# Kernel optimization log

Hardware: AMD Instinct MI355X
Metric: run time of the kernel (lower is better)

Reference implementation:

```python
import jax, jax.numpy as jnp
import numpy as np

N = 100000   # nodes
E = 1600000  # edges
G = 512      # graphs in batch
F_IN = 128
H = 128
F_OUT = 1


def setup_inputs() -> dict:
    key = jax.random.key(0)
    ks = jax.random.split(key, 12)
    x = jax.random.normal(ks[0], (N, F_IN), dtype=jnp.float32)
    src = jax.random.randint(ks[1], (E,), 0, N, dtype=jnp.int32)
    dst = jax.random.randint(ks[2], (E,), 0, N, dtype=jnp.int32)
    node2graph = jnp.sort(jax.random.randint(ks[3], (N,), 0, G, dtype=jnp.int32))
    s_in = 1.0 / np.sqrt(F_IN)
    s_h = 1.0 / np.sqrt(H)
    W0 = jax.random.normal(ks[4], (F_IN, H), dtype=jnp.float32) * s_in
    b0 = jnp.zeros((H,), dtype=jnp.float32)
    W1 = jax.random.normal(ks[5], (H, H), dtype=jnp.float32) * s_h
    b1 = jnp.zeros((H,), dtype=jnp.float32)
    W2 = jax.random.normal(ks[6], (H, H), dtype=jnp.float32) * s_h
    b2 = jnp.zeros((H,), dtype=jnp.float32)
    Wm1 = jax.random.normal(ks[7], (H, H), dtype=jnp.float32) * s_h
    bm1 = jnp.zeros((H,), dtype=jnp.float32)
    Wm2 = jax.random.normal(ks[8], (H, F_OUT), dtype=jnp.float32) * s_h
    bm2 = jnp.zeros((F_OUT,), dtype=jnp.float32)
    return {"x": x, "src": src, "dst": dst, "node2graph": node2graph,
            "W0": W0, "b0": b0, "W1": W1, "b1": b1, "W2": W2, "b2": b2,
            "Wm1": Wm1, "bm1": bm1, "Wm2": Wm2, "bm2": bm2}


def _degree_norms(src, dst):
    ones = jnp.ones((E,), dtype=jnp.float32)
    out_deg = jax.ops.segment_sum(ones, src, num_segments=N)
    in_deg = jax.ops.segment_sum(ones, dst, num_segments=N)
    norm_out = jax.lax.rsqrt(jnp.maximum(out_deg, 1.0))  # [N]
    norm_in = jax.lax.rsqrt(jnp.maximum(in_deg, 1.0))    # [N]
    return norm_out, norm_in


def _graph_conv(x, src, dst, norm_out, norm_in, W, b):
    # DGL GraphConv, norm='both', in_feats <= out_feats path:
    # aggregate normalized src features, then linear + activation.
    xs = x * norm_out[:, None]
    msg = xs[src]                                         # [E, H] gather
    agg = jax.ops.segment_sum(msg, dst, num_segments=N)   # [N, H] scatter-add
    agg = agg * norm_in[:, None]
    return jax.nn.relu(agg @ W + b)


def reference(x, src, dst, node2graph, W0, b0, W1, b1, W2, b2, Wm1, bm1, Wm2, bm2):
    norm_out, norm_in = _degree_norms(src, dst)
    h = _graph_conv(x, src, dst, norm_out, norm_in, W0, b0)
    h = _graph_conv(h, src, dst, norm_out, norm_in, W1, b1)
    h = _graph_conv(h, src, dst, norm_out, norm_in, W2, b2)
    # sum_nodes readout per graph
    g = jax.ops.segment_sum(h, node2graph, num_segments=G)  # [G, H]
    # MLP head: Linear -> ReLU -> Linear
    return jax.nn.relu(g @ Wm1 + bm1) @ Wm2 + bm2           # [G, 1]
```

## Files before the change

kernel.cpp:

```cpp
#include <hip/hip_runtime.h>

#define NN 100000
#define NE 1600000
#define NG 512
#define HD 128

#define NBK 196
#define CHUNK 5120
#define NC 313
#define LH (2 * NBK * NC)

typedef _Float16 h8 __attribute__((ext_vector_type(8)));
typedef float f32x4 __attribute__((ext_vector_type(4)));

__global__ __launch_bounds__(512) void k_hist(const int* __restrict__ src,
                                              const int* __restrict__ dst,
                                              int* __restrict__ H,
                                              const float* __restrict__ W0,
                                              const float* __restrict__ W1,
                                              const float* __restrict__ W2,
                                              _Float16* __restrict__ Bt) {
    if (blockIdx.x >= NC) {
        int i = (blockIdx.x - NC) * 512 + threadIdx.x;
        int w = i >> 14;
        int rem = i & 16383;
        int n = rem >> 7;
        int k = rem & 127;
        const float* W = (w == 0) ? W0 : ((w == 1) ? W1 : W2);
        Bt[i] = (_Float16)W[k * 128 + n];
        return;
    }
    __shared__ int hd[NBK], hs[NBK];
    int c = blockIdx.x;
    for (int i = threadIdx.x; i < NBK; i += 512) { hd[i] = 0; hs[i] = 0; }
    __syncthreads();
    int e0 = c * CHUNK;
    int e1 = e0 + CHUNK; if (e1 > NE) e1 = NE;
    for (int e = e0 + threadIdx.x; e < e1; e += 512) {
        atomicAdd(&hd[dst[e] >> 9], 1);
        atomicAdd(&hs[src[e] >> 9], 1);
    }
    __syncthreads();
    for (int i = threadIdx.x; i < NBK; i += 512) {
        H[i * NC + c] = hd[i];
        H[NBK * NC + i * NC + c] = hs[i];
    }
}

__global__ __launch_bounds__(256) void k_scan1g(int* __restrict__ H,
                                                int* __restrict__ bsum, int L) {
    __shared__ int s[256];
    int i = blockIdx.x * 256 + threadIdx.x;
    int v = (i < L) ? H[i] : 0;
    s[threadIdx.x] = v;
    __syncthreads();
    for (int off = 1; off < 256; off <<= 1) {
        int t = (threadIdx.x >= off) ? s[threadIdx.x - off] : 0;
        __syncthreads();
        s[threadIdx.x] += t;
        __syncthreads();
    }
    if (i < L) H[i] = s[threadIdx.x] - v;
    if (threadIdx.x == 255) bsum[blockIdx.x] = s[255];
}

__global__ __launch_bounds__(256) void k_scan3g(int* __restrict__ H,
                                                const int* __restrict__ bsum,
                                                int L, int nb) {
    __shared__ int sb[512];
    __shared__ int tmp2[256];
    int t = threadIdx.x;
    int b0 = (2 * t < nb) ? bsum[2 * t] : 0;
    int b1 = (2 * t + 1 < nb) ? bsum[2 * t + 1] : 0;
    int pair = b0 + b1;
    tmp2[t] = pair;
    __syncthreads();
    for (int off = 1; off < 256; off <<= 1) {
        int v2 = (t >= off) ? tmp2[t - off] : 0;
        __syncthreads();
        tmp2[t] += v2;
        __syncthreads();
    }
    int ex = tmp2[t] - pair;
    sb[2 * t] = ex;
    sb[2 * t + 1] = ex + b0;
    __syncthreads();
    int i = blockIdx.x * 256 + t;
    if (i < L) H[i] += sb[i >> 8];
}

__global__ __launch_bounds__(512) void k_scatter(const int* __restrict__ src,
                                                 const int* __restrict__ dst,
                                                 const int* __restrict__ H,
                                                 int* __restrict__ dpart,
                                                 unsigned short* __restrict__ spart) {
    __shared__ int cd[NBK], cs[NBK];
    int c = blockIdx.x;
    for (int i = threadIdx.x; i < NBK; i += 512) {
        cd[i] = H[i * NC + c];
        cs[i] = H[NBK * NC + i * NC + c] - NE;
    }
    __syncthreads();
    int e0 = c * CHUNK;
    int e1 = e0 + CHUNK; if (e1 > NE) e1 = NE;
    for (int e = e0 + threadIdx.x; e < e1; e += 512) {
        int s = src[e], d = dst[e];
        int pd = atomicAdd(&cd[d >> 9], 1);
        dpart[pd] = s | ((d & 511) << 17);
        int ps = atomicAdd(&cs[s >> 9], 1);
        spart[ps] = (unsigned short)(s & 511);
    }
}

__global__ __launch_bounds__(512) void k_bucket(const int* __restrict__ dpart,
                                                const unsigned short* __restrict__ spart,
                                                const int* __restrict__ H,
                                                int* __restrict__ offs,
                                                int* __restrict__ csr,
                                                float* __restrict__ ni,
                                                float* __restrict__ no) {
    __shared__ int deg[512];
    __shared__ int cur[512];
    __shared__ int tmp[512];
    int b = blockIdx.x;
    bool isDst = (b < NBK);
    int bb = isDst ? b : b - NBK;
    int start, end;
    if (isDst) {
        start = H[bb * NC];
        end = (bb + 1 < NBK) ? H[(bb + 1) * NC] : NE;
    } else {
        start = H[NBK * NC + bb * NC] - NE;
        end = (bb + 1 < NBK) ? H[NBK * NC + (bb + 1) * NC] - NE : NE;
    }
    int t = threadIdx.x;
    deg[t] = 0;
    __syncthreads();
    if (isDst) {
        for (int i = start + t; i < end; i += 512)
            atomicAdd(&deg[(dpart[i] >> 17) & 511], 1);
    } else {
        for (int i = start + t; i < end; i += 512)
            atomicAdd(&deg[spart[i]], 1);
    }
    __syncthreads();
    int vb = bb * 512;
    if (!isDst) {
        int v = vb + t;
        if (v < NN) no[v] = rsqrtf(fmaxf((float)deg[t], 1.0f));
        return;
    }
    int a = deg[t];
    tmp[t] = a;
    __syncthreads();
    for (int off = 1; off < 512; off <<= 1) {
        int v2 = (t >= off) ? tmp[t - off] : 0;
        __syncthreads();
        tmp[t] += v2;
        __syncthreads();
    }
    cur[t] = start + tmp[t] - a;
    {
        int v = vb + t;
        if (v < NN) {
            offs[v] = cur[t];
            ni[v] = rsqrtf(fmaxf((float)a, 1.0f));
        }
    }
    if (b == NBK - 1 && t == 0) offs[NN] = NE;
    __syncthreads();
    for (int i = start + t; i < end; i += 512) {
        int pk = dpart[i];
        int p = atomicAdd(&cur[(pk >> 17) & 511], 1);
        csr[p] = pk & 0x1FFFF;
    }
}

template <typename TA>
__global__ __launch_bounds__(256) void k_gemm_mfma(const TA* __restrict__ A,
                                                   const _Float16* __restrict__ Bt,
                                                   const float* __restrict__ no,
                                                   _Float16* __restrict__ Zh,
                                                   int nrows) {
    __shared__ _Float16 Bs[128 * 136];
    int tid = threadIdx.x;
    {
        const h8* B8 = (const h8*)Bt;
        h8* Bs8 = (h8*)Bs;
        for (int i = tid; i < 2048; i += 256) {
            int n = i >> 4, c = i & 15;
            Bs8[n * 17 + c] = B8[i];
        }
    }

    int wave = tid >> 6;
    int lane = tid & 63;
    int m16 = lane & 15;
    int quad = lane >> 4;
    int rowbase = blockIdx.x * 64 + wave * 16;
    int row = rowbase + m16;
    bool valid = row < nrows;

    h8 afrag[4];
    if (valid) {
        if constexpr (sizeof(TA) == 2) {
            const h8* Arow = (const h8*)(A + (size_t)row * 128);
#pragma unroll
            for (int kk = 0; kk < 4; kk++) afrag[kk] = Arow[kk * 4 + quad];
        } else {
            const float4* Arow = (const float4*)(A + (size_t)row * 128);
#pragma unroll
            for (int kk = 0; kk < 4; kk++) {
                float4 lo = Arow[kk * 8 + quad * 2];
                float4 hi = Arow[kk * 8 + quad * 2 + 1];
                h8 a;
                a[0] = (_Float16)lo.x; a[1] = (_Float16)lo.y;
                a[2] = (_Float16)lo.z; a[3] = (_Float16)lo.w;
                a[4] = (_Float16)hi.x; a[5] = (_Float16)hi.y;
                a[6] = (_Float16)hi.z; a[7] = (_Float16)hi.w;
                afrag[kk] = a;
            }
        }
    } else {
#pragma unroll
        for (int kk = 0; kk < 4; kk++) {
            h8 a;
#pragma unroll
            for (int j = 0; j < 8; j++) a[j] = (_Float16)0.f;
            afrag[kk] = a;
        }
    }

    __syncthreads();

    f32x4 acc[8];
#pragma unroll
    for (int nt = 0; nt < 8; nt++) acc[nt] = (f32x4){0.f, 0.f, 0.f, 0.f};

    const h8* Bs8 = (const h8*)Bs;
#pragma unroll
    for (int nt = 0; nt < 8; nt++) {
        const h8* Bp = Bs8 + (size_t)(nt * 16 + m16) * 17;
#pragma unroll
        for (int kk = 0; kk < 4; kk++) {
            acc[nt] = __builtin_amdgcn_mfma_f32_16x16x32_f16(afrag[kk], Bp[kk * 4 + quad],
                                                             acc[nt], 0, 0, 0);
        }
    }

    float nor[4];
#pragma unroll
    for (int r = 0; r < 4; r++) {
        int grow = rowbase + quad * 4 + r;
        nor[r] = (grow < nrows) ? no[grow] : 0.f;
    }

    __syncthreads();
    {
        int lr0 = wave * 16 + quad * 4;
#pragma unroll
        for (int nt = 0; nt < 8; nt++) {
#pragma unroll
            for (int r = 0; r < 4; r++) {
                Bs[(size_t)(lr0 + r) * 136 + nt * 16 + m16] =
                    (_Float16)(acc[nt][r] * nor[r]);
            }
        }
    }
    __syncthreads();

    int blockrow0 = blockIdx.x * 64;
    for (int i = tid; i < 1024; i += 256) {
        int r = i >> 4, cch = i & 15;
        int grow = blockrow0 + r;
        if (grow < nrows) {
            h8 val = *(const h8*)&Bs[(size_t)r * 136 + cch * 8];
            *(h8*)&Zh[(size_t)grow * 128 + cch * 8] = val;
        }
    }
}

__global__ __launch_bounds__(256) void k_agg(const h8* __restrict__ Zh,
                                             const int* __restrict__ offs,
                                             const int* __restrict__ csr,
                                             const float* __restrict__ ni,
                                             const float* __restrict__ b,
                                             h8* __restrict__ H16) {
    int v = blockIdx.x * 16 + (threadIdx.x >> 4);
    int c = threadIdx.x & 15;
    int s = offs[v];
    int e = offs[v + 1];
    float a0[8], a1[8];
#pragma unroll
    for (int j = 0; j < 8; j++) { a0[j] = 0.f; a1[j] = 0.f; }
    int i = s;
    for (; i + 4 <= e; i += 4) {
        int u0 = csr[i];
        int u1 = csr[i + 1];
        int u2 = csr[i + 2];
        int u3 = csr[i + 3];
        h8 z0 = Zh[(size_t)u0 * 16 + c];
        h8 z1 = Zh[(size_t)u1 * 16 + c];
        h8 z2 = Zh[(size_t)u2 * 16 + c];
        h8 z3 = Zh[(size_t)u3 * 16 + c];
#pragma unroll
        for (int j = 0; j < 8; j++) {
            a0[j] += (float)z0[j] + (float)z1[j];
            a1[j] += (float)z2[j] + (float)z3[j];
        }
    }
    for (; i < e; i++) {
        int u = csr[i];
        h8 z = Zh[(size_t)u * 16 + c];
#pragma unroll
        for (int j = 0; j < 8; j++) a0[j] += (float)z[j];
    }
    float niv = ni[v];
    const float* bb = b + c * 8;
    h8 r;
#pragma unroll
    for (int j = 0; j < 8; j++)
        r[j] = (_Float16)fmaxf((a0[j] + a1[j]) * niv + bb[j], 0.f);
    H16[(size_t)v * 16 + c] = r;
}

__global__ __launch_bounds__(256) void k_readhead(const h8* __restrict__ H8,
                                                  const int* __restrict__ n2g,
                                                  const float* __restrict__ Wm1,
                                                  const float* __restrict__ bm1,
                                                  const float* __restrict__ Wm2,
                                                  const float* __restrict__ bm2,
                                                  float* __restrict__ out) {
    __shared__ float red[256 * 8];
    __shared__ float gs[128];
    __shared__ float red2[128];
    int gi = blockIdx.x;
    int t = threadIdx.x;
    int slot = t >> 4;
    int c = t & 15;

    int lo = 0, hi = NN;
    while (lo < hi) { int mid = (lo + hi) >> 1; if (n2g[mid] < gi) lo = mid + 1; else hi = mid; }
    int s = lo;
    hi = NN;
    while (lo < hi) { int mid = (lo + hi) >> 1; if (n2g[mid] < gi + 1) lo = mid + 1; else hi = mid; }
    int e = lo;

    float acc[8];
#pragma unroll
    for (int j = 0; j < 8; j++) acc[j] = 0.f;
    for (int v = s + slot; v < e; v += 16) {
        h8 z = H8[(size_t)v * 16 + c];
#pragma unroll
        for (int j = 0; j < 8; j++) acc[j] += (float)z[j];
    }
#pragma unroll
    for (int j = 0; j < 8; j++) red[t * 8 + j] = acc[j];
    __syncthreads();
    for (int off = 8; off >= 1; off >>= 1) {
        if (slot < off) {
#pragma unroll
            for (int j = 0; j < 8; j++)
                red[t * 8 + j] += red[(t + off * 16) * 8 + j];
        }
        __syncthreads();
    }
    if (slot == 0) {
#pragma unroll
        for (int j = 0; j < 8; j++) gs[c * 8 + j] = red[t * 8 + j];
    }
    __syncthreads();

    if (t < 128) {
        float a = bm1[t];
        for (int k = 0; k < 128; k++) a += gs[k] * Wm1[k * 128 + t];
        red2[t] = fmaxf(a, 0.f) * Wm2[t];
    }
    __syncthreads();
    for (int s2 = 64; s2 > 0; s2 >>= 1) {
        if (t < s2) red2[t] += red2[t + s2];
        __syncthreads();
    }
    if (t == 0) out[gi] = red2[0] + bm2[0];
}

extern "C" void kernel_launch(void* const* d_in, const int* in_sizes, int n_in,
                              void* d_out, int out_size, void* d_ws, size_t ws_size,
                              hipStream_t stream) {
    const float* x   = (const float*)d_in[0];
    const int*   src = (const int*)d_in[1];
    const int*   dst = (const int*)d_in[2];
    const int*   n2g = (const int*)d_in[3];
    const float* W0  = (const float*)d_in[4];
    const float* b0  = (const float*)d_in[5];
    const float* W1  = (const float*)d_in[6];
    const float* b1  = (const float*)d_in[7];
    const float* W2  = (const float*)d_in[8];
    const float* b2  = (const float*)d_in[9];
    const float* Wm1 = (const float*)d_in[10];
    const float* bm1 = (const float*)d_in[11];
    const float* Wm2 = (const float*)d_in[12];
    const float* bm2 = (const float*)d_in[13];
    float* out = (float*)d_out;

    char* p = (char*)d_ws;
    auto carve = [&](size_t bytes) -> char* {
        char* r = p;
        p += (bytes + 255) & ~(size_t)255;
        return r;
    };
    _Float16* zh  = (_Float16*)carve((size_t)NN * HD * 2);
    _Float16* h16 = (_Float16*)carve((size_t)NN * HD * 2);
    _Float16* Bt  = (_Float16*)carve((size_t)3 * 128 * 128 * 2);
    float* no     = (float*)carve((size_t)NN * 4);
    float* ni     = (float*)carve((size_t)NN * 4);
    int*   offs   = (int*)carve((size_t)(NN + 1) * 4);
    int*   csr    = (int*)carve((size_t)NE * 4);
    int*   Hh     = (int*)carve((size_t)LH * 4);
    int*   bsum   = (int*)carve((size_t)512 * 4);
    int*   dpart  = (int*)carve((size_t)NE * 4);
    unsigned short* spart = (unsigned short*)carve((size_t)NE * 2);

    int scan_blocks = (LH + 255) / 256;
    k_hist<<<NC + 96, 512, 0, stream>>>(src, dst, Hh, W0, W1, W2, Bt);
    k_scan1g<<<scan_blocks, 256, 0, stream>>>(Hh, bsum, LH);
    k_scan3g<<<scan_blocks, 256, 0, stream>>>(Hh, bsum, LH, scan_blocks);
    k_scatter<<<NC, 512, 0, stream>>>(src, dst, Hh, dpart, spart);
    k_bucket<<<2 * NBK, 512, 0, stream>>>(dpart, spart, Hh, offs, csr, ni, no);

    int gemm_blocks = (NN + 63) / 64;
    int agg_blocks  = NN / 16;

    k_gemm_mfma<float><<<gemm_blocks, 256, 0, stream>>>(x, Bt, no, zh, NN);
    k_agg<<<agg_blocks, 256, 0, stream>>>((const h8*)zh, offs, csr, ni, b0, (h8*)h16);
    k_gemm_mfma<_Float16><<<gemm_blocks, 256, 0, stream>>>(h16, Bt + 16384, no, zh, NN);
    k_agg<<<agg_blocks, 256, 0, stream>>>((const h8*)zh, offs, csr, ni, b1, (h8*)h16);
    k_gemm_mfma<_Float16><<<gemm_blocks, 256, 0, stream>>>(h16, Bt + 32768, no, zh, NN);
    k_agg<<<agg_blocks, 256, 0, stream>>>((const h8*)zh, offs, csr, ni, b2, (h8*)h16);

    k_readhead<<<NG, 256, 0, stream>>>((const h8*)h16, n2g, Wm1, bm1, Wm2, bm2, out);
}
```

Measured before the change: 391.9 us.

## Build CSR with global atomic degree count and direct fill; split readout

Replaces the two-level bucketed partition (histogram, scan, scatter, bucket sort) with a direct CSR build: global atomics count in- and out-degrees per node, a node-level scan yields offsets and norms, and a fill kernel scatters sources using per-node atomic cursors. This removes several passes over the edge arrays and the intermediate partition buffers, at the cost of heavy global atomic contention and a non-deterministic neighbour order within each row. The readout is split into a four-way partitioned graph sum using float atomics plus a separate MLP head kernel, which raises parallelism for the per-graph reduction. A zeroing kernel is added to clear the degree counters and the graph accumulator.

```diff
diff --git a/kernel.cpp b/kernel.cpp
--- a/kernel.cpp
+++ b/kernel.cpp
@@ -5,23 +5,27 @@
 #define NG 512
 #define HD 128
 
-#define NBK 196
-#define CHUNK 5120
-#define NC 313
-#define LH (2 * NBK * NC)
-
 typedef _Float16 h8 __attribute__((ext_vector_type(8)));
 typedef float f32x4 __attribute__((ext_vector_type(4)));
 
-__global__ __launch_bounds__(512) void k_hist(const int* __restrict__ src,
-                                              const int* __restrict__ dst,
-                                              int* __restrict__ H,
-                                              const float* __restrict__ W0,
-                                              const float* __restrict__ W1,
-                                              const float* __restrict__ W2,
-                                              _Float16* __restrict__ Bt) {
-    if (blockIdx.x >= NC) {
-        int i = (blockIdx.x - NC) * 512 + threadIdx.x;
+#define NDEG 1563
+
+__global__ __launch_bounds__(256) void k_zero(int4* __restrict__ z, int n4) {
+    int i = blockIdx.x * 256 + threadIdx.x;
+    int stride = gridDim.x * 256;
+    for (; i < n4; i += stride) z[i] = make_int4(0, 0, 0, 0);
+}
+
+__global__ __launch_bounds__(512) void k_deg(const int* __restrict__ src,
+                                             const int* __restrict__ dst,
+                                             int* __restrict__ ind,
+                                             int* __restrict__ outd,
+                                             const float* __restrict__ W0,
+                                             const float* __restrict__ W1,
+                                             const float* __restrict__ W2,
+                                             _Float16* __restrict__ Bt) {
+    if (blockIdx.x >= NDEG) {
+        int i = (blockIdx.x - NDEG) * 512 + threadIdx.x;
         int w = i >> 14;
         int rem = i & 16383;
         int n = rem >> 7;
@@ -30,28 +34,26 @@
         Bt[i] = (_Float16)W[k * 128 + n];
         return;
     }
-    __shared__ int hd[NBK], hs[NBK];
-    int c = blockIdx.x;
-    for (int i = threadIdx.x; i < NBK; i += 512) { hd[i] = 0; hs[i] = 0; }
-    __syncthreads();
-    int e0 = c * CHUNK;
-    int e1 = e0 + CHUNK; if (e1 > NE) e1 = NE;
-    for (int e = e0 + threadIdx.x; e < e1; e += 512) {
-        atomicAdd(&hd[dst[e] >> 9], 1);
-        atomicAdd(&hs[src[e] >> 9], 1);
-    }
-    __syncthreads();
-    for (int i = threadIdx.x; i < NBK; i += 512) {
-        H[i * NC + c] = hd[i];
-        H[NBK * NC + i * NC + c] = hs[i];
-    }
-}
-
-__global__ __launch_bounds__(256) void k_scan1g(int* __restrict__ H,
-                                                int* __restrict__ bsum, int L) {
+    int e = blockIdx.x * 512 + threadIdx.x;
+    int stride = NDEG * 512;
+    for (; e < NE; e += stride) {
+        atomicAdd(&outd[src[e]], 1);
+        atomicAdd(&ind[dst[e]], 1);
+    }
+}
+
+__global__ __launch_bounds__(256) void k_scan1n(int* __restrict__ ind,
+                                                const int* __restrict__ outd,
+                                                float* __restrict__ ni,
+                                                float* __restrict__ no,
+                                                int* __restrict__ bsum) {
     __shared__ int s[256];
     int i = blockIdx.x * 256 + threadIdx.x;
-    int v = (i < L) ? H[i] : 0;
+    int v = (i < NN) ? ind[i] : 0;
+    if (i < NN) {
+        ni[i] = rsqrtf(fmaxf((float)v, 1.0f));
+        no[i] = rsqrtf(fmaxf((float)outd[i], 1.0f));
+    }
     s[threadIdx.x] = v;
     __syncthreads();
     for (int off = 1; off < 256; off <<= 1) {
@@ -60,13 +62,13 @@
         s[threadIdx.x] += t;
         __syncthreads();
     }
-    if (i < L) H[i] = s[threadIdx.x] - v;
+    if (i < NN) ind[i] = s[threadIdx.x] - v;
     if (threadIdx.x == 255) bsum[blockIdx.x] = s[255];
 }
 
-__global__ __launch_bounds__(256) void k_scan3g(int* __restrict__ H,
+__global__ __launch_bounds__(256) void k_scan3c(int* __restrict__ H,
                                                 const int* __restrict__ bsum,
-                                                int L, int nb) {
+                                                int* __restrict__ cur, int nb) {
     __shared__ int sb[512];
     __shared__ int tmp2[256];
     int t = threadIdx.x;
@@ -86,93 +88,24 @@
     sb[2 * t + 1] = ex + b0;
     __syncthreads();
     int i = blockIdx.x * 256 + t;
-    if (i < L) H[i] += sb[i >> 8];
-}
-
-__global__ __launch_bounds__(512) void k_scatter(const int* __restrict__ src,
-                                                 const int* __restrict__ dst,
-                                                 const int* __restrict__ H,
-                                                 int* __restrict__ dpart,
-                                                 unsigned short* __restrict__ spart) {
-    __shared__ int cd[NBK], cs[NBK];
-    int c = blockIdx.x;
-    for (int i = threadIdx.x; i < NBK; i += 512) {
-        cd[i] = H[i * NC + c];
-        cs[i] = H[NBK * NC + i * NC + c] - NE;
-    }
-    __syncthreads();
-    int e0 = c * CHUNK;
-    int e1 = e0 + CHUNK; if (e1 > NE) e1 = NE;
-    for (int e = e0 + threadIdx.x; e < e1; e += 512) {
-        int s = src[e], d = dst[e];
-        int pd = atomicAdd(&cd[d >> 9], 1);
-        dpart[pd] = s | ((d & 511) << 17);
-        int ps = atomicAdd(&cs[s >> 9], 1);
-        spart[ps] = (unsigned short)(s & 511);
-    }
-}
-
-__global__ __launch_bounds__(512) void k_bucket(const int* __restrict__ dpart,
-                                                const unsigned short* __restrict__ spart,
-                                                const int* __restrict__ H,
-                                                int* __restrict__ offs,
-                                                int* __restrict__ csr,
-                                                float* __restrict__ ni,
-                                                float* __restrict__ no) {
-    __shared__ int deg[512];
-    __shared__ int cur[512];
-    __shared__ int tmp[512];
-    int b = blockIdx.x;
-    bool isDst = (b < NBK);
-    int bb = isDst ? b : b - NBK;
-    int start, end;
-    if (isDst) {
-        start = H[bb * NC];
-        end = (bb + 1 < NBK) ? H[(bb + 1) * NC] : NE;
-    } else {
-        start = H[NBK * NC + bb * NC] - NE;
-        end = (bb + 1 < NBK) ? H[NBK * NC + (bb + 1) * NC] - NE : NE;
-    }
-    int t = threadIdx.x;
-    deg[t] = 0;
-    __syncthreads();
-    if (isDst) {
-        for (int i = start + t; i < end; i += 512)
-            atomicAdd(&deg[(dpart[i] >> 17) & 511], 1);
-    } else {
-        for (int i = start + t; i < end; i += 512)
-            atomicAdd(&deg[spart[i]], 1);
-    }
-    __syncthreads();
-    int vb = bb * 512;
-    if (!isDst) {
-        int v = vb + t;
-        if (v < NN) no[v] = rsqrtf(fmaxf((float)deg[t], 1.0f));
-        return;
-    }
-    int a = deg[t];
-    tmp[t] = a;
-    __syncthreads();
-    for (int off = 1; off < 512; off <<= 1) {
-        int v2 = (t >= off) ? tmp[t - off] : 0;
-        __syncthreads();
-        tmp[t] += v2;
-        __syncthreads();
-    }
-    cur[t] = start + tmp[t] - a;
-    {
-        int v = vb + t;
-        if (v < NN) {
-            offs[v] = cur[t];
-            ni[v] = rsqrtf(fmaxf((float)a, 1.0f));
-        }
-    }
-    if (b == NBK - 1 && t == 0) offs[NN] = NE;
-    __syncthreads();
-    for (int i = start + t; i < end; i += 512) {
-        int pk = dpart[i];
-        int p = atomicAdd(&cur[(pk >> 17) & 511], 1);
-        csr[p] = pk & 0x1FFFF;
+    if (i < NN) {
+        int val = H[i] + sb[i >> 8];
+        H[i] = val;
+        cur[i] = val;
+    }
+    if (blockIdx.x == 0 && t == 0) H[NN] = NE;
+}
+
+__global__ __launch_bounds__(256) void k_fill(const int* __restrict__ src,
+                                              const int* __restrict__ dst,
+                                              int* __restrict__ cur,
+                                              int* __restrict__ csr) {
+    int e = blockIdx.x * 256 + threadIdx.x;
+    int stride = gridDim.x * 256;
+    for (; e < NE; e += stride) {
+        int d = dst[e];
+        int p = atomicAdd(&cur[d], 1);
+        csr[p] = src[e];
     }
 }
 
@@ -324,17 +257,12 @@
     H16[(size_t)v * 16 + c] = r;
 }
 
-__global__ __launch_bounds__(256) void k_readhead(const h8* __restrict__ H8,
-                                                  const int* __restrict__ n2g,
-                                                  const float* __restrict__ Wm1,
-                                                  const float* __restrict__ bm1,
-                                                  const float* __restrict__ Wm2,
-                                                  const float* __restrict__ bm2,
-                                                  float* __restrict__ out) {
+__global__ __launch_bounds__(256) void k_gsum(const h8* __restrict__ H8,
+                                              const int* __restrict__ n2g,
+                                              float* __restrict__ gbuf) {
     __shared__ float red[256 * 8];
-    __shared__ float gs[128];
-    __shared__ float red2[128];
-    int gi = blockIdx.x;
+    int gi = blockIdx.x >> 2;
+    int part = blockIdx.x & 3;
     int t = threadIdx.x;
     int slot = t >> 4;
     int c = t & 15;
@@ -349,7 +277,7 @@
     float acc[8];
 #pragma unroll
     for (int j = 0; j < 8; j++) acc[j] = 0.f;
-    for (int v = s + slot; v < e; v += 16) {
+    for (int v = s + part * 16 + slot; v < e; v += 64) {
         h8 z = H8[(size_t)v * 16 + c];
 #pragma unroll
         for (int j = 0; j < 8; j++) acc[j] += (float)z[j];
@@ -367,15 +295,26 @@
     }
     if (slot == 0) {
 #pragma unroll
-        for (int j = 0; j < 8; j++) gs[c * 8 + j] = red[t * 8 + j];
-    }
-    __syncthreads();
-
-    if (t < 128) {
-        float a = bm1[t];
-        for (int k = 0; k < 128; k++) a += gs[k] * Wm1[k * 128 + t];
-        red2[t] = fmaxf(a, 0.f) * Wm2[t];
-    }
+        for (int j = 0; j < 8; j++)
+            atomicAdd(&gbuf[gi * 128 + c * 8 + j], red[t * 8 + j]);
+    }
+}
+
+__global__ __launch_bounds__(128) void k_head(const float* __restrict__ gbuf,
+                                              const float* __restrict__ Wm1,
+                                              const float* __restrict__ bm1,
+                                              const float* __restrict__ Wm2,
+                                              const float* __restrict__ bm2,
+                                              float* __restrict__ out) {
+    __shared__ float gs[128];
+    __shared__ float red2[128];
+    int gi = blockIdx.x;
+    int t = threadIdx.x;
+    gs[t] = gbuf[gi * 128 + t];
+    __syncthreads();
+    float a = bm1[t];
+    for (int k = 0; k < 128; k++) a += gs[k] * Wm1[k * 128 + t];
+    red2[t] = fmaxf(a, 0.f) * Wm2[t];
     __syncthreads();
     for (int s2 = 64; s2 > 0; s2 >>= 1) {
         if (t < s2) red2[t] += red2[t + s2];
@@ -414,19 +353,22 @@
     _Float16* Bt  = (_Float16*)carve((size_t)3 * 128 * 128 * 2);
     float* no     = (float*)carve((size_t)NN * 4);
     float* ni     = (float*)carve((size_t)NN * 4);
+    char* zbase   = p;
     int*   offs   = (int*)carve((size_t)(NN + 1) * 4);
+    int*   outd   = (int*)carve((size_t)NN * 4);
+    float* gbuf   = (float*)carve((size_t)NG * 128 * 4);
+    size_t zbytes = (size_t)(p - zbase);
+    int*   cur    = (int*)carve((size_t)NN * 4);
     int*   csr    = (int*)carve((size_t)NE * 4);
-    int*   Hh     = (int*)carve((size_t)LH * 4);
     int*   bsum   = (int*)carve((size_t)512 * 4);
-    int*   dpart  = (int*)carve((size_t)NE * 4);
-    unsigned short* spart = (unsigned short*)carve((size_t)NE * 2);
-
-    int scan_blocks = (LH + 255) / 256;
-    k_hist<<<NC + 96, 512, 0, stream>>>(src, dst, Hh, W0, W1, W2, Bt);
-    k_scan1g<<<scan_blocks, 256, 0, stream>>>(Hh, bsum, LH);
-    k_scan3g<<<scan_blocks, 256, 0, stream>>>(Hh, bsum, LH, scan_blocks);
-    k_scatter<<<NC, 512, 0, stream>>>(src, dst, Hh, dpart, spart);
-    k_bucket<<<2 * NBK, 512, 0, stream>>>(dpart, spart, Hh, offs, csr, ni, no);
+
+    int scan_blocks = (NN + 255) / 256;
+
+    k_zero<<<256, 256, 0, stream>>>((int4*)zbase, (int)(zbytes / 16));
+    k_deg<<<NDEG + 96, 512, 0, stream>>>(src, dst, offs, outd, W0, W1, W2, Bt);
+    k_scan1n<<<scan_blocks, 256, 0, stream>>>(offs, outd, ni, no, bsum);
+    k_scan3c<<<scan_blocks, 256, 0, stream>>>(offs, bsum, cur, scan_blocks);
+    k_fill<<<3125, 256, 0, stream>>>(src, dst, cur, csr);
 
     int gemm_blocks = (NN + 63) / 64;
     int agg_blocks  = NN / 16;
@@ -438,5 +380,6 @@
     k_gemm_mfma<_Float16><<<gemm_blocks, 256, 0, stream>>>(h16, Bt + 32768, no, zh, NN);
     k_agg<<<agg_blocks, 256, 0, stream>>>((const h8*)zh, offs, csr, ni, b2, (h8*)h16);
 
-    k_readhead<<<NG, 256, 0, stream>>>((const h8*)h16, n2g, Wm1, bm1, Wm2, bm2, out);
-}
+    k_gsum<<<NG * 4, 256, 0, stream>>>((const h8*)h16, n2g, gbuf);
+    k_head<<<NG, 128, 0, stream>>>(gbuf, Wm1, bm1, Wm2, bm2, out);
+}
```

After: 606.4 us. 54.7% more time.
